# Performance work log

Hardware: AMD Instinct MI355X
Metric: run time of the kernel (lower is better)

The kernel has to match this reference:

```python
import jax, jax.numpy as jnp
import numpy as np
from jax import lax

D_MODEL = 512
KERNEL = 17
DILATION = 1
MLP_MULT = 4
EPS = 1e-6


def rmsnorm(x, w):
    # x: [B,T,C]; RMSNorm: x * rsqrt(mean(x^2) + eps) * w
    ms = jnp.mean(x * x, axis=-1, keepdims=True)
    return x * lax.rsqrt(ms + EPS) * w


def causal_dwconv(x, w, dilation):
    # x: [B,T,C], w: [C,K]. Equivalent math to the FFT path in the torch code:
    # y[b,t,c] = sum_k w[c,k] * x[b, t - dilation*(K-1) + dilation*k, c] (zeros off left edge)
    B, T, C = x.shape
    K = w.shape[1]
    left_pad = dilation * (K - 1)
    lhs = jnp.transpose(x, (0, 2, 1))          # [B,C,T]
    rhs = w[:, None, :]                        # [C,1,K] depthwise
    y = lax.conv_general_dilated(
        lhs, rhs,
        window_strides=(1,),
        padding=[(left_pad, 0)],
        rhs_dilation=(dilation,),
        dimension_numbers=('NCH', 'OIH', 'NCH'),
        feature_group_count=C,
    )                                          # [B,C,T]
    return jnp.transpose(y, (0, 2, 1))


def setup_inputs() -> dict:
    key = jax.random.key(0)
    ks = jax.random.split(key, 8)
    B, T, d = 4, 16384, D_MODEL
    h = MLP_MULT * d
    scale = lambda fan_in: 1.0 / np.sqrt(fan_in)
    return {
        'x': jax.random.normal(ks[0], (B, T, d), jnp.float32),
        'ln1_w': jnp.ones((d,), jnp.float32),
        'gate_w': jax.random.normal(ks[1], (d, d), jnp.float32) * scale(d),
        'conv_w': jax.random.uniform(ks[2], (d, KERNEL), jnp.float32,
                                     -scale(KERNEL), scale(KERNEL)),
        'proj_w': jax.random.normal(ks[3], (d, d), jnp.float32) * scale(d),
        'ln2_w': jnp.ones((d,), jnp.float32),
        'mlp_w1': jax.random.normal(ks[4], (d, h), jnp.float32) * scale(d),
        'mlp_w2': jax.random.normal(ks[5], (h, d), jnp.float32) * scale(h),
    }


def reference(x, ln1_w, gate_w, conv_w, proj_w, ln2_w, mlp_w1, mlp_w2):
    # Gated depthwise causal conv branch
    hn = rmsnorm(x, ln1_w)
    g = jax.nn.sigmoid(jnp.einsum('btd,de->bte', hn, gate_w))
    hc = causal_dwconv(hn, conv_w, DILATION)
    x = x + jnp.einsum('btd,de->bte', g * hc, proj_w)
    # MLP branch
    hn2 = rmsnorm(x, ln2_w)
    mid = jax.nn.gelu(jnp.einsum('btd,dh->bth', hn2, mlp_w1))
    x = x + jnp.einsum('bth,hd->btd', mid, mlp_w2)
    return x
```

## Files before the change

### kernel.cpp

```cpp
#include <hip/hip_runtime.h>
#include <hip/hip_bf16.h>
#include <cstdint>
#include <cstddef>

typedef __attribute__((ext_vector_type(8))) short short8;
typedef __attribute__((ext_vector_type(4))) short short4v;
typedef __attribute__((ext_vector_type(4))) float floatx4;

#define D_MODEL 512
#define HDIM    2048
#define TSEQ    16384
#define NTOK    65536

__device__ __forceinline__ float bf2f(short s) {
  union { unsigned u; float f; } v; v.u = ((unsigned)(unsigned short)s) << 16; return v.f;
}
__device__ __forceinline__ short f2bf(float f) {
  union { float fv; unsigned u; } v; v.fv = f;
  unsigned u = v.u;
  u += 0x7FFFu + ((u >> 16) & 1u);
  return (short)(u >> 16);
}
__device__ __forceinline__ void gload_lds16(const void* g, void* l) {
  __builtin_amdgcn_global_load_lds((const __attribute__((address_space(1))) void*)g,
                                   (__attribute__((address_space(3))) void*)l, 16, 0, 0);
}

__global__ void wt_transpose(const float* __restrict__ W, short* __restrict__ Wt,
                             const int K, const int N) {
  __shared__ float t[64][65];
  const int tid = threadIdx.x;
  const long k0 = (long)blockIdx.x * 64;
  const long n0 = (long)blockIdx.y * 64;
  const int rr = tid >> 4;
  const int cc = (tid & 15) * 4;
#pragma unroll
  for (int i = 0; i < 4; ++i) {
    const int r = rr + i * 16;
    const float4 v = *(const float4*)(W + (k0 + r) * N + n0 + cc);
    t[r][cc + 0] = v.x; t[r][cc + 1] = v.y; t[r][cc + 2] = v.z; t[r][cc + 3] = v.w;
  }
  __syncthreads();
#pragma unroll
  for (int i = 0; i < 4; ++i) {
    const int n = rr + i * 16;
    short4v o;
    o[0] = f2bf(t[cc + 0][n]);
    o[1] = f2bf(t[cc + 1][n]);
    o[2] = f2bf(t[cc + 2][n]);
    o[3] = f2bf(t[cc + 3][n]);
    *(short4v*)(Wt + (n0 + n) * K + k0 + cc) = o;
  }
}

__global__ void convw_transpose(const float* __restrict__ cw, float* __restrict__ wT) {
  const int idx = blockIdx.x * 256 + threadIdx.x;
  if (idx >= 17 * D_MODEL) return;
  const int k = idx / D_MODEL;
  const int c = idx % D_MODEL;
  wT[idx] = cw[c * 17 + k];
}

__global__ void rmsnorm_kernel(const float* __restrict__ x, const float* __restrict__ w,
                               short* __restrict__ outp) {
  const int lane = threadIdx.x & 63;
  const long row = (long)blockIdx.x * 4 + (threadIdx.x >> 6);
  const float* xr = x + row * D_MODEL + lane * 8;
  const float4 a = *(const float4*)xr;
  const float4 b = *(const float4*)(xr + 4);
  float ss = a.x * a.x + a.y * a.y + a.z * a.z + a.w * a.w
           + b.x * b.x + b.y * b.y + b.z * b.z + b.w * b.w;
#pragma unroll
  for (int m = 32; m; m >>= 1) ss += __shfl_xor(ss, m);
  const float scale = rsqrtf(ss * (1.0f / D_MODEL) + 1e-6f);
  const float4 wa = *(const float4*)(w + lane * 8);
  const float4 wb = *(const float4*)(w + lane * 8 + 4);
  short8 o;
  o[0] = f2bf(a.x * scale * wa.x);
  o[1] = f2bf(a.y * scale * wa.y);
  o[2] = f2bf(a.z * scale * wa.z);
  o[3] = f2bf(a.w * scale * wa.w);
  o[4] = f2bf(b.x * scale * wb.x);
  o[5] = f2bf(b.y * scale * wb.y);
  o[6] = f2bf(b.z * scale * wb.z);
  o[7] = f2bf(b.w * scale * wb.w);
  *(short8*)(outp + row * D_MODEL + lane * 8) = o;
}

__global__ void dwconv_kernel(const short* __restrict__ hn, const float* __restrict__ wT,
                              short* __restrict__ hc) {
  const int tid = threadIdx.x;
  const int chunk = tid & 63;
  const long row = (long)blockIdx.x * 4 + (tid >> 6);
  const int t = (int)(row & (TSEQ - 1));
  const int c0 = chunk * 8;
  float acc[8];
#pragma unroll
  for (int j = 0; j < 8; ++j) acc[j] = 0.f;
  const int kmin = (t >= 16) ? 0 : (16 - t);
  for (int k = kmin; k < 17; ++k) {
    const short8 h = *(const short8*)(hn + (row - 16 + k) * D_MODEL + c0);
    const float* wp = wT + k * D_MODEL + c0;
    const float4 w0 = *(const float4*)(wp);
    const float4 w1 = *(const float4*)(wp + 4);
    acc[0] += bf2f(h[0]) * w0.x;
    acc[1] += bf2f(h[1]) * w0.y;
    acc[2] += bf2f(h[2]) * w0.z;
    acc[3] += bf2f(h[3]) * w0.w;
    acc[4] += bf2f(h[4]) * w1.x;
    acc[5] += bf2f(h[5]) * w1.y;
    acc[6] += bf2f(h[6]) * w1.z;
    acc[7] += bf2f(h[7]) * w1.w;
  }
  short8 o;
#pragma unroll
  for (int j = 0; j < 8; ++j) o[j] = f2bf(acc[j]);
  *(short8*)(hc + row * D_MODEL + c0) = o;
}

#define PHASE_BAR() __builtin_amdgcn_s_barrier()
#define LGKM0() { asm volatile("s_waitcnt lgkmcnt(0)" ::: "memory"); __builtin_amdgcn_sched_barrier(0); }
#define VMC4()  { asm volatile("s_waitcnt vmcnt(4)" ::: "memory"); __builtin_amdgcn_sched_barrier(0); }
#define VMC0()  { asm volatile("s_waitcnt vmcnt(0)" ::: "memory"); __builtin_amdgcn_sched_barrier(0); }

template <int EPI>
__global__ __launch_bounds__(512, 2)
void gemm256(const short* __restrict__ A, const short* __restrict__ Bt,
             const int K, const int N, const int nbn,
             const void* __restrict__ aux, void* __restrict__ outp) {
  __shared__ short Alds[2 * 2 * 128 * 64];
  __shared__ short Blds[2 * 2 * 128 * 64];
  const int tid = threadIdx.x;
  const int lane = tid & 63;
  const int w = tid >> 6;
  const int wm = w >> 2;
  const int wn = w & 3;

  const int nwg = gridDim.x;
  const int cpx = nwg >> 3;
  const int bid = blockIdx.x;
  const int wid = (bid & 7) * cpx + (bid >> 3);
  const long brow = (long)(wid / nbn) * 256;
  const long bcol = (long)(wid % nbn) * 256;

  floatx4 acc[8][4];
#pragma unroll
  for (int i = 0; i < 8; ++i)
#pragma unroll
    for (int j = 0; j < 4; ++j) acc[i][j] = {0.f, 0.f, 0.f, 0.f};

  short8 af[4][2];
  short8 bfr[4][2];

  const int chunkx = (lane & 7) ^ (lane >> 3);
  const short* gA = A + (brow + w * 8 + (lane >> 3)) * (long)K + chunkx * 8;
  const short* gB = Bt + (bcol + w * 8 + (lane >> 3)) * (long)K + chunkx * 8;
  const int kchunk = lane >> 4;

#define STGA(half, BUF, koff)                                                  \
  { _Pragma("unroll")                                                          \
    for (int j = 0; j < 2; ++j)                                                \
      gload_lds16(gA + ((half) * 128 + j * 64) * (long)K + (koff),             \
                  &Alds[(((BUF) * 2 + (half)) * 128 + j * 64 + w * 8) * 64]); }
#define STGB(half, BUF, koff)                                                  \
  { _Pragma("unroll")                                                          \
    for (int j = 0; j < 2; ++j)                                                \
      gload_lds16(gB + ((half) * 128 + j * 64) * (long)K + (koff),             \
                  &Blds[(((BUF) * 2 + (half)) * 128 + j * 64 + w * 8) * 64]); }

#define LDA4(mbase, BUF)                                                       \
  { _Pragma("unroll")                                                          \
    for (int mi = 0; mi < 4; ++mi)                                             \
      _Pragma("unroll")                                                        \
      for (int ks = 0; ks < 2; ++ks) {                                         \
        const int r = ((mbase) + mi) * 16 + (lane & 15);                       \
        const int c = (ks * 4 + kchunk) ^ (r & 7);                             \
        af[mi][ks] = *(const short8*)(&Alds[(((BUF) * 2 + wm) * 128 + r) * 64 + c * 8]); \
      } }
#define LDB2(nbase, BUF)                                                       \
  { _Pragma("unroll")                                                          \
    for (int nn = 0; nn < 2; ++nn)                                             \
      _Pragma("unroll")                                                        \
      for (int ks = 0; ks < 2; ++ks) {                                         \
        const int r = (wn & 1) * 64 + ((nbase) + nn) * 16 + (lane & 15);       \
        const int c = (ks * 4 + kchunk) ^ (r & 7);                             \
        bfr[(nbase) + nn][ks] = *(const short8*)(&Blds[(((BUF) * 2 + (wn >> 1)) * 128 + r) * 64 + c * 8]); \
      } }

#define MMACL(mbase, nbase)                                                    \
  { __builtin_amdgcn_s_setprio(1);                                             \
    _Pragma("unroll")                                                          \
    for (int mi = 0; mi < 4; ++mi)                                             \
      _Pragma("unroll")                                                        \
      for (int nn = 0; nn < 2; ++nn)                                           \
        _Pragma("unroll")                                                      \
        for (int ks = 0; ks < 2; ++ks)                                         \
          acc[(mbase) + mi][(nbase) + nn] = __builtin_amdgcn_mfma_f32_16x16x32_bf16( \
              af[mi][ks], bfr[(nbase) + nn][ks], acc[(mbase) + mi][(nbase) + nn], 0, 0, 0); \
    __builtin_amdgcn_s_setprio(0); }

#define TILE(BUF, DOST01, DOST23, W4, W0, kA, kB)                              \
  {                                                                            \
                                                                       \
    LDA4(0, BUF); LDB2(0, BUF);                                                \
    if (DOST01) STGA(0, (BUF) ^ 1, kA);                                        \
    PHASE_BAR(); LGKM0(); MMACL(0, 0); PHASE_BAR();                            \
                                                                       \
    LDB2(2, BUF);                                                              \
    if (DOST01) STGA(1, (BUF) ^ 1, kA);                                        \
    PHASE_BAR(); LGKM0(); MMACL(0, 2); PHASE_BAR();                            \
                                                                       \
    LDA4(4, BUF);                                                              \
    if (DOST23) STGB(0, BUF, kB);                                              \
    PHASE_BAR(); LGKM0(); MMACL(4, 0); PHASE_BAR();                            \
                                                                       \
    if (DOST23) STGB(1, BUF, kB);                                              \
    if (W4) VMC4();                                                            \
    if (W0) VMC0();                                                            \
    PHASE_BAR(); MMACL(4, 2); PHASE_BAR();                                     \
  }

  STGB(0, 0, 0); STGB(1, 0, 0); STGA(0, 0, 0); STGA(1, 0, 0);
  STGB(0, 1, 64); STGB(1, 1, 64);
  VMC4(); PHASE_BAR();

  const int nkt = K >> 6;
  int kA = 64, kB = 128;
  for (int t = 0; t < nkt - 2; t += 2) {
    TILE(0, 1, 1, 1, 0, kA, kB); kA += 64; kB += 64;
    TILE(1, 1, 1, 1, 0, kA, kB); kA += 64; kB += 64;
  }
  TILE(0, 1, 0, 0, 1, kA, 0);
  TILE(1, 0, 0, 0, 0, 0, 0);

#undef TILE
#undef MMACL
#undef LDA4
#undef LDB2
#undef STGA
#undef STGB

#pragma unroll
  for (int mi = 0; mi < 8; ++mi) {
#pragma unroll
    for (int ni = 0; ni < 4; ++ni) {
      const long gc = bcol + wn * 64 + ni * 16 + (lane & 15);
      const long r0 = brow + wm * 128 + mi * 16 + (lane >> 4) * 4;
#pragma unroll
      for (int j = 0; j < 4; ++j) {
        const long r = r0 + j;
        const float v = acc[mi][ni][j];
        const long idx = r * (long)N + gc;
        if (EPI == 0) {
          const float hcv = bf2f(((const short*)aux)[idx]);
          const float g = 1.f / (1.f + __expf(-v));
          ((short*)outp)[idx] = f2bf(g * hcv);
        } else if (EPI == 1) {
          ((float*)outp)[idx] = ((const float*)aux)[idx] + v;
        } else if (EPI == 2) {
          const float x3 = v * v * v;
          const float z = 0.7978845608028654f * (v + 0.044715f * x3);
          const float th = 1.f - 2.f / (__expf(2.f * z) + 1.f);
          ((short*)outp)[idx] = f2bf(0.5f * v * (1.f + th));
        } else {
          ((float*)outp)[idx] += v;
        }
      }
    }
  }
}

extern "C" void kernel_launch(void* const* d_in, const int* in_sizes, int n_in,
                              void* d_out, int out_size, void* d_ws, size_t ws_size,
                              hipStream_t stream) {
  const float* x      = (const float*)d_in[0];
  const float* ln1_w  = (const float*)d_in[1];
  const float* gate_w = (const float*)d_in[2];
  const float* conv_w = (const float*)d_in[3];
  const float* proj_w = (const float*)d_in[4];
  const float* ln2_w  = (const float*)d_in[5];
  const float* mlp_w1 = (const float*)d_in[6];
  const float* mlp_w2 = (const float*)d_in[7];
  float* out = (float*)d_out;
  char* ws = (char*)d_ws;

  short* hn      = (short*)(ws + 0);
  short* hc      = (short*)(ws + 67108864L);
  short* mid     = (short*)(ws + 134217728L);
  short* gate_wt = (short*)(ws + 402653184L);
  short* proj_wt = (short*)(ws + 403177472L);
  short* w1t     = (short*)(ws + 403701760L);
  short* w2t     = (short*)(ws + 405798912L);
  float* convwT  = (float*)(ws + 407896064L);

  const dim3 b256(256);
  const dim3 b512(512);

  wt_transpose<<<dim3(8, 8),  b256, 0, stream>>>(gate_w, gate_wt, 512, 512);
  wt_transpose<<<dim3(8, 8),  b256, 0, stream>>>(proj_w, proj_wt, 512, 512);
  wt_transpose<<<dim3(8, 32), b256, 0, stream>>>(mlp_w1, w1t, 512, 2048);
  wt_transpose<<<dim3(32, 8), b256, 0, stream>>>(mlp_w2, w2t, 2048, 512);
  convw_transpose<<<34, b256, 0, stream>>>(conv_w, convwT);

  rmsnorm_kernel<<<NTOK / 4, b256, 0, stream>>>(x, ln1_w, hn);
  dwconv_kernel<<<NTOK / 4, b256, 0, stream>>>(hn, convwT, hc);
  gemm256<0><<<256 * 2, b512, 0, stream>>>(hn, gate_wt, 512, 512, 2, hc, hc);
  gemm256<1><<<256 * 2, b512, 0, stream>>>(hc, proj_wt, 512, 512, 2, x, out);
  rmsnorm_kernel<<<NTOK / 4, b256, 0, stream>>>(out, ln2_w, hn);
  gemm256<2><<<256 * 8, b512, 0, stream>>>(hn, w1t, 512, 2048, 8, nullptr, mid);
  gemm256<3><<<256 * 2, b512, 0, stream>>>(mid, w2t, 2048, 512, 2, nullptr, out);
}
```

Baseline: 808.0 us.

## Use inline-asm LDS reads with immediate offsets, reorder waits, simplify epilogue indexing

Replaces the compiler-generated swizzled LDS fragment loads with inline ds_read_b128 instructions that use precomputed per-lane base addresses and immediate offsets, cutting address arithmetic and VGPR pressure. Moves the vmcnt wait after the last MFMA cluster of each tile so global-to-LDS loads overlap more compute before the barrier. Switches epilogue indexing to 32-bit ints with reordered loops to reduce 64-bit address math. Inline asm outputs lack explicit lgkmcnt dependency tracking, so correctness relies on the existing manual waits. The 32-bit indexing assumes the index stays below 2^31.

```diff
diff --git a/kernel.cpp b/kernel.cpp
--- a/kernel.cpp
+++ b/kernel.cpp
@@ -122,6 +122,8 @@
 #define LGKM0() { asm volatile("s_waitcnt lgkmcnt(0)" ::: "memory"); __builtin_amdgcn_sched_barrier(0); }
 #define VMC4()  { asm volatile("s_waitcnt vmcnt(4)" ::: "memory"); __builtin_amdgcn_sched_barrier(0); }
 #define VMC0()  { asm volatile("s_waitcnt vmcnt(0)" ::: "memory"); __builtin_amdgcn_sched_barrier(0); }
+#define DSR1(dst, addr, imm) \
+  asm volatile("ds_read_b128 %0, %1 offset:%2" : "=v"(dst) : "v"(addr), "i"(imm))
 
 template <int EPI>
 __global__ __launch_bounds__(512, 2)
@@ -157,6 +159,16 @@
   const short* gB = Bt + (bcol + w * 8 + (lane >> 3)) * (long)K + chunkx * 8;
   const int kchunk = lane >> 4;
 
+  const unsigned Abase = (unsigned)(uintptr_t)(__attribute__((address_space(3))) short*)Alds;
+  const unsigned Bbase = (unsigned)(uintptr_t)(__attribute__((address_space(3))) short*)Blds;
+  const unsigned lanelo = (unsigned)((lane & 15) * 128);
+  const unsigned c0t = (unsigned)(((0 + kchunk) ^ (lane & 7)) * 16);
+  const unsigned c1t = (unsigned)(((4 + kchunk) ^ (lane & 7)) * 16);
+  const unsigned adrA0 = Abase + (unsigned)(wm * 16384) + lanelo + c0t;
+  const unsigned adrA1 = Abase + (unsigned)(wm * 16384) + lanelo + c1t;
+  const unsigned adrB0 = Bbase + (unsigned)((wn >> 1) * 16384 + (wn & 1) * 8192) + lanelo + c0t;
+  const unsigned adrB1 = Bbase + (unsigned)((wn >> 1) * 16384 + (wn & 1) * 8192) + lanelo + c1t;
+
 #define STGA(half, BUF, koff)                                                  \
   { _Pragma("unroll")                                                          \
     for (int j = 0; j < 2; ++j)                                                \
@@ -168,24 +180,20 @@
       gload_lds16(gB + ((half) * 128 + j * 64) * (long)K + (koff),             \
                   &Blds[(((BUF) * 2 + (half)) * 128 + j * 64 + w * 8) * 64]); }
 
-#define LDA4(mbase, BUF)                                                       \
-  { _Pragma("unroll")                                                          \
-    for (int mi = 0; mi < 4; ++mi)                                             \
-      _Pragma("unroll")                                                        \
-      for (int ks = 0; ks < 2; ++ks) {                                         \
-        const int r = ((mbase) + mi) * 16 + (lane & 15);                       \
-        const int c = (ks * 4 + kchunk) ^ (r & 7);                             \
-        af[mi][ks] = *(const short8*)(&Alds[(((BUF) * 2 + wm) * 128 + r) * 64 + c * 8]); \
-      } }
-#define LDB2(nbase, BUF)                                                       \
-  { _Pragma("unroll")                                                          \
-    for (int nn = 0; nn < 2; ++nn)                                             \
-      _Pragma("unroll")                                                        \
-      for (int ks = 0; ks < 2; ++ks) {                                         \
-        const int r = (wn & 1) * 64 + ((nbase) + nn) * 16 + (lane & 15);       \
-        const int c = (ks * 4 + kchunk) ^ (r & 7);                             \
-        bfr[(nbase) + nn][ks] = *(const short8*)(&Blds[(((BUF) * 2 + (wn >> 1)) * 128 + r) * 64 + c * 8]); \
-      } }
+#define LDA4(mbase, BUF) {                                                     \
+    DSR1(af[0][0], adrA0, (BUF)*32768 + ((mbase)+0)*2048);                     \
+    DSR1(af[0][1], adrA1, (BUF)*32768 + ((mbase)+0)*2048);                     \
+    DSR1(af[1][0], adrA0, (BUF)*32768 + ((mbase)+1)*2048);                     \
+    DSR1(af[1][1], adrA1, (BUF)*32768 + ((mbase)+1)*2048);                     \
+    DSR1(af[2][0], adrA0, (BUF)*32768 + ((mbase)+2)*2048);                     \
+    DSR1(af[2][1], adrA1, (BUF)*32768 + ((mbase)+2)*2048);                     \
+    DSR1(af[3][0], adrA0, (BUF)*32768 + ((mbase)+3)*2048);                     \
+    DSR1(af[3][1], adrA1, (BUF)*32768 + ((mbase)+3)*2048); }
+#define LDB2(nbase, BUF) {                                                     \
+    DSR1(bfr[(nbase)+0][0], adrB0, (BUF)*32768 + ((nbase)+0)*2048);            \
+    DSR1(bfr[(nbase)+0][1], adrB1, (BUF)*32768 + ((nbase)+0)*2048);            \
+    DSR1(bfr[(nbase)+1][0], adrB0, (BUF)*32768 + ((nbase)+1)*2048);            \
+    DSR1(bfr[(nbase)+1][1], adrB1, (BUF)*32768 + ((nbase)+1)*2048); }
 
 #define MMACL(mbase, nbase)                                                    \
   { __builtin_amdgcn_s_setprio(1);                                             \
@@ -215,9 +223,10 @@
     PHASE_BAR(); LGKM0(); MMACL(4, 0); PHASE_BAR();                            \
                                                                        \
     if (DOST23) STGB(1, BUF, kB);                                              \
+    PHASE_BAR(); MMACL(4, 2);                                                  \
     if (W4) VMC4();                                                            \
     if (W0) VMC0();                                                            \
-    PHASE_BAR(); MMACL(4, 2); PHASE_BAR();                                     \
+    PHASE_BAR();                                                               \
   }
 
   STGB(0, 0, 0); STGB(1, 0, 0); STGA(0, 0, 0); STGA(1, 0, 0);
@@ -242,15 +251,15 @@
 
 #pragma unroll
   for (int mi = 0; mi < 8; ++mi) {
-#pragma unroll
-    for (int ni = 0; ni < 4; ++ni) {
-      const long gc = bcol + wn * 64 + ni * 16 + (lane & 15);
-      const long r0 = brow + wm * 128 + mi * 16 + (lane >> 4) * 4;
-#pragma unroll
-      for (int j = 0; j < 4; ++j) {
-        const long r = r0 + j;
+    const int r0 = (int)brow + wm * 128 + mi * 16 + (lane >> 4) * 4;
+#pragma unroll
+    for (int j = 0; j < 4; ++j) {
+      const int rb = (r0 + j) * N;
+      const int gcb = (int)bcol + wn * 64 + (lane & 15);
+#pragma unroll
+      for (int ni = 0; ni < 4; ++ni) {
+        const int idx = rb + gcb + ni * 16;
         const float v = acc[mi][ni][j];
-        const long idx = r * (long)N + gc;
         if (EPI == 0) {
           const float hcv = bf2f(((const short*)aux)[idx]);
           const float g = 1.f / (1.f + __expf(-v));
```

Result: faster. 695.9 us (-13.9%).
